# Optimization experiments

Measured on AMD Instinct MI355X. Metric: run time of the kernel, lower is better.

Reference implementation:

```python
import jax, jax.numpy as jnp
import numpy as np
import math

H = 8
E = 512
D_K = E // H
NEG = -1000000000.0
# last (and only surviving) row of dist_bar: one threshold per head
DIST_BAR = np.array([0.2, 0.3, 0.4, 0.5, 0.6, 0.7, 0.8, 0.9], dtype=np.float32)


def setup_inputs() -> dict:
    key = jax.random.key(0)
    ks = jax.random.split(key, 12)
    B, N = 8, 1024
    s = 1.0 / math.sqrt(E)
    inp = {
        "query": jax.random.normal(ks[0], (B, N, E), jnp.float32),
        "key": jax.random.normal(ks[1], (B, N, E), jnp.float32),
        "value": jax.random.normal(ks[2], (B, N, E), jnp.float32),
        "dist": jax.random.uniform(ks[3], (B, 1, N, N), jnp.float32),
        "mask": jnp.ones((B, N, N), jnp.int32),
        "Wq": jax.random.normal(ks[4], (E, E), jnp.float32) * s,
        "bq": jnp.zeros((E,), jnp.float32),
        "Wk": jax.random.normal(ks[5], (E, E), jnp.float32) * s,
        "bk": jnp.zeros((E,), jnp.float32),
        "Wv": jax.random.normal(ks[6], (E, E), jnp.float32) * s,
        "bv": jnp.zeros((E,), jnp.float32),
        "Wo": jax.random.normal(ks[7], (E, E), jnp.float32) * s,
        "bo": jnp.zeros((E,), jnp.float32),
    }
    return inp


def reference(query, key, value, dist, mask, Wq, bq, Wk, bk, Wv, bv, Wo, bo):
    B, N, _ = query.shape
    # project and split heads: [B, H, N, D_K]
    def heads(x, W, b):
        return (x @ W.T + b).reshape(B, N, H, D_K).transpose(0, 2, 1, 3)
    q = heads(query, Wq, bq)
    k = heads(key, Wk, bk)
    v = heads(value, Wv, bv)
    scores = jnp.einsum("bhqd,bhkd->bhqk", q, k) / math.sqrt(D_K)
    # padding mask: [B,N,N] -> [B,1,N,N]
    scores = jnp.where(mask[:, None, :, :] == 0, NEG, scores)
    # per-head distance mask: dist [B,1,N,N] < thr[h] -> [B,H,N,N]
    thr = jnp.asarray(DIST_BAR)[None, :, None, None]
    dmask = dist < thr
    # first row/col (global atom) always attend
    dmask = dmask.at[:, :, 0, :].set(True).at[:, :, :, 0].set(True)
    scores = jnp.where(dmask, scores, NEG)
    p = jax.nn.softmax(scores, axis=-1)
    out = jnp.einsum("bhqk,bhkd->bhqd", p, v)  # [B,H,N,D_K]
    out = out.transpose(0, 2, 1, 3).reshape(B, N, H * D_K)
    return out @ Wo.T + bo
```

## Files before the change

### kernel.cpp

```cpp
#include <hip/hip_runtime.h>
#include <stdint.h>


typedef __attribute__((ext_vector_type(8))) short short8;
typedef __attribute__((ext_vector_type(4))) float floatx4;

#define MFMA16(a, b, c) __builtin_amdgcn_mfma_f32_16x16x32_bf16((a), (b), (c), 0, 0, 0)

static __device__ __forceinline__ unsigned short f2bf(float f) {
  union { float f; unsigned u; } v; v.f = f;
  unsigned r = v.u + 0x7fffu + ((v.u >> 16) & 1u);
  return (unsigned short)(r >> 16);
}

static __device__ __forceinline__ void gload_lds16(const void* g, void* l) {
  __builtin_amdgcn_global_load_lds((const __attribute__((address_space(1))) unsigned int*)g,
                                   (__attribute__((address_space(3))) unsigned int*)l,
                                   16, 0, 0);
}
static __device__ __forceinline__ int xsw(int row) { return (row & 3) ^ ((row >> 2) & 3); }

__global__ void prep_kernel(const float* __restrict__ dist, const int* __restrict__ mask,
                            unsigned char* __restrict__ codesP,
                            const float* __restrict__ Wq, const float* __restrict__ Wk,
                            const float* __restrict__ Wv, const float* __restrict__ Wo,
                            unsigned short* __restrict__ o0, unsigned short* __restrict__ o1,
                            unsigned short* __restrict__ o2, unsigned short* __restrict__ o3,
                            const float* __restrict__ Qf, const float* __restrict__ Kf,
                            const float* __restrict__ Vf,
                            unsigned short* __restrict__ Qb, unsigned short* __restrict__ Kb,
                            unsigned short* __restrict__ Vb) {
  const int tid = threadIdx.x;
  const unsigned bx = blockIdx.x;
  if (bx >= 3072) {
    int j = bx - 3072;
    int arr = j >> 11;
    const float* s = (arr == 0) ? Qf : (arr == 1) ? Kf : Vf;
    unsigned short* d = (arr == 0) ? Qb : (arr == 1) ? Kb : Vb;
    int idx = (j & 2047) * 256 + tid;
    float4 v0 = ((const float4*)s)[idx * 2];
    float4 v1 = ((const float4*)s)[idx * 2 + 1];
    short8 o;
    o[0] = (short)f2bf(v0.x); o[1] = (short)f2bf(v0.y);
    o[2] = (short)f2bf(v0.z); o[3] = (short)f2bf(v0.w);
    o[4] = (short)f2bf(v1.x); o[5] = (short)f2bf(v1.y);
    o[6] = (short)f2bf(v1.z); o[7] = (short)f2bf(v1.w);
    *(short8*)(d + (size_t)idx * 8) = o;
    return;
  }
  if (bx >= 2048) {
    int i = (bx - 2048) * 256 + tid;
    int w = i >> 16, loc = i & 65535;
    const float* s = (w == 0) ? Wq : (w == 1) ? Wk : (w == 2) ? Wv : Wo;
    unsigned short* d = (w == 0) ? o0 : (w == 1) ? o1 : (w == 2) ? o2 : o3;
    float4 v = ((const float4*)s)[loc];
    ushort4 o;
    o.x = f2bf(v.x); o.y = f2bf(v.y); o.z = f2bf(v.z); o.w = f2bf(v.w);
    ((ushort4*)d)[loc] = o;
    return;
  }
  __shared__ __align__(16) unsigned char cbuf[4096];
  const int bc = bx;
  const int b = bc >> 8;
  const int rg = (bc >> 3) & 31;
  const int kt = bc & 7;
  const int row_local = tid >> 3;
  const int colseg = (tid & 7) * 16;
  const int row = rg * 32 + row_local;
  const int st = row_local >> 4;
  const int c = row_local & 15;
  const int ci = tid & 7;
  const size_t ibase = ((size_t)b << 20) + (size_t)row * 1024 + kt * 128 + colseg;
  float4 d4[4]; int4 m4[4];
#pragma unroll
  for (int g = 0; g < 4; g++) {
    d4[g] = ((const float4*)(dist + ibase))[g];
    m4[g] = ((const int4*)(mask + ibase))[g];
  }
#pragma unroll
  for (int hi = 0; hi < 4; hi++) {
    float dvv[4] = {d4[hi].x, d4[hi].y, d4[hi].z, d4[hi].w};
    int mvv[4] = {m4[hi].x, m4[hi].y, m4[hi].z, m4[hi].w};
    unsigned pack = 0;
#pragma unroll
    for (int r = 0; r < 4; r++) {
      int col = kt * 128 + colseg + hi * 4 + r;
      float d = dvv[r];
      int hmin = (d >= 0.2f) + (d >= 0.3f) + (d >= 0.4f) + (d >= 0.5f) +
                 (d >= 0.6f) + (d >= 0.7f) + (d >= 0.8f) + (d >= 0.9f);
      unsigned cc = (unsigned)hmin;
      if (row == 0 || col == 0) cc = 0;
      if (mvv[r] == 0) cc = 9;
      pack |= cc << (r * 8);
    }
    *(unsigned*)&cbuf[(hi * 16 + c) * 64 + st * 32 + ci * 4] = pack;
  }
  __syncthreads();
  *(uint4*)&codesP[(size_t)bc * 4096 + tid * 16] = *(const uint4*)&cbuf[tid * 16];
}

__global__ __launch_bounds__(256) void qkv_gemm(
    const unsigned short* __restrict__ Aq, const unsigned short* __restrict__ Ak,
    const unsigned short* __restrict__ Av,
    const unsigned short* __restrict__ Wqp, const unsigned short* __restrict__ Wkp,
    const unsigned short* __restrict__ Wvp,
    const float* __restrict__ bq, const float* __restrict__ bk, const float* __restrict__ bv,
    unsigned short* __restrict__ Qh, unsigned short* __restrict__ Kh,
    unsigned short* __restrict__ Vt) {
  const int z = blockIdx.z;
  const unsigned short* A = (z == 0) ? Aq : (z == 1) ? Ak : Av;
  const unsigned short* W = (z == 0) ? Wqp : (z == 1) ? Wkp : Wvp;
  const float* bias = (z == 0) ? bq : (z == 1) ? bk : bv;
  unsigned short* O = (z == 0) ? Qh : (z == 1) ? Kh : Vt;

  __shared__ __align__(16) short As[128 * 32];
  __shared__ __align__(16) short Bs[128 * 32];
  const int tid = threadIdx.x;
  const int lane = tid & 63;
  const int wave = tid >> 6;
  const int c = lane & 15;
  const int q = lane >> 4;
  const int m0 = blockIdx.x * 128;
  const int n0 = blockIdx.y * 128;
  const int wr = (wave >> 1) * 64;
  const int wc = (wave & 1) * 64;

  floatx4 acc[4][4];
#pragma unroll
  for (int i = 0; i < 4; i++)
#pragma unroll
    for (int j = 0; j < 4; j++) acc[i][j] = (floatx4)(0.0f);

  for (int k0 = 0; k0 < 512; k0 += 32) {
    __syncthreads();
#pragma unroll
    for (int it = 0; it < 2; it++) {
      int slot = wave * 128 + it * 64 + lane;
      int arow = slot >> 2, ach = slot & 3;
      int g = ach ^ xsw(arow);
      gload_lds16(A + (size_t)(m0 + arow) * 512 + k0 + g * 8,
                  &As[(size_t)(wave * 128 + it * 64) * 8]);
      gload_lds16(W + (size_t)(n0 + arow) * 512 + k0 + g * 8,
                  &Bs[(size_t)(wave * 128 + it * 64) * 8]);
    }
    __syncthreads();

    short8 af[4], bfv[4];
#pragma unroll
    for (int i = 0; i < 4; i++) {
      int row = wr + i * 16 + c;
      af[i] = *(const short8*)(&As[row * 32 + (q ^ xsw(row)) * 8]);
    }
#pragma unroll
    for (int j = 0; j < 4; j++) {
      int row = wc + j * 16 + c;
      bfv[j] = *(const short8*)(&Bs[row * 32 + (q ^ xsw(row)) * 8]);
    }
#pragma unroll
    for (int i = 0; i < 4; i++)
#pragma unroll
      for (int j = 0; j < 4; j++)
        acc[i][j] = MFMA16(af[i], bfv[j], acc[i][j]);
  }

#pragma unroll
  for (int i = 0; i < 4; i++) {
    int gm0 = m0 + wr + i * 16 + q * 4;
#pragma unroll
    for (int j = 0; j < 4; j++) {
      int gn = n0 + wc + j * 16 + c;
      float bb = bias[gn];
      int h = gn >> 6, d = gn & 63;
      if (z == 2) {
        int b = gm0 >> 10, n = gm0 & 1023;
        ushort4 pk;
#pragma unroll
        for (int r = 0; r < 4; r++) pk[r] = f2bf(acc[i][j][r] + bb);
        *(ushort4*)(&Vt[(((size_t)(b * 8 + h) * 64 + d) << 10) + n]) = pk;
      } else {
#pragma unroll
        for (int r = 0; r < 4; r++) {
          int m = gm0 + r;
          int b = m >> 10, n = m & 1023;
          O[((((size_t)(b * 8 + h)) << 10) + n) * 64 + d] = f2bf(acc[i][j][r] + bb);
        }
      }
    }
  }
}

__global__ __launch_bounds__(256) void out_gemm(const unsigned short* __restrict__ A,
                                                const unsigned short* __restrict__ W,
                                                const float* __restrict__ bias,
                                                float* __restrict__ Out) {
  __shared__ __align__(16) short As[64 * 32];
  __shared__ __align__(16) short Bs[128 * 32];
  const int tid = threadIdx.x;
  const int lane = tid & 63;
  const int wave = tid >> 6;
  const int c = lane & 15;
  const int q = lane >> 4;
  const int m0 = blockIdx.x * 64;
  const int n0 = blockIdx.y * 128;
  const int wr = (wave >> 1) * 32;
  const int wc = (wave & 1) * 64;

  floatx4 acc[2][4];
#pragma unroll
  for (int i = 0; i < 2; i++)
#pragma unroll
    for (int j = 0; j < 4; j++) acc[i][j] = (floatx4)(0.0f);

  for (int k0 = 0; k0 < 512; k0 += 32) {
    __syncthreads();
    {
      int slot = wave * 64 + lane;
      int arow = slot >> 2, ach = slot & 3;
      int g = ach ^ xsw(arow);
      gload_lds16(A + (size_t)(m0 + arow) * 512 + k0 + g * 8, &As[(size_t)(wave * 64) * 8]);
    }
#pragma unroll
    for (int it = 0; it < 2; it++) {
      int slot = wave * 128 + it * 64 + lane;
      int brow = slot >> 2, bch = slot & 3;
      int g = bch ^ xsw(brow);
      gload_lds16(W + (size_t)(n0 + brow) * 512 + k0 + g * 8,
                  &Bs[(size_t)(wave * 128 + it * 64) * 8]);
    }
    __syncthreads();

    short8 af[2], bfv[4];
#pragma unroll
    for (int i = 0; i < 2; i++) {
      int row = wr + i * 16 + c;
      af[i] = *(const short8*)(&As[row * 32 + (q ^ xsw(row)) * 8]);
    }
#pragma unroll
    for (int j = 0; j < 4; j++) {
      int row = wc + j * 16 + c;
      bfv[j] = *(const short8*)(&Bs[row * 32 + (q ^ xsw(row)) * 8]);
    }
#pragma unroll
    for (int i = 0; i < 2; i++)
#pragma unroll
      for (int j = 0; j < 4; j++)
        acc[i][j] = MFMA16(af[i], bfv[j], acc[i][j]);
  }

#pragma unroll
  for (int i = 0; i < 2; i++) {
    int gm0 = m0 + wr + i * 16 + q * 4;
#pragma unroll
    for (int j = 0; j < 4; j++) {
      int gn = n0 + wc + j * 16 + c;
      float bb = bias[gn];
#pragma unroll
      for (int r = 0; r < 4; r++)
        Out[(size_t)(gm0 + r) * 512 + gn] = acc[i][j][r] + bb;
    }
  }
}

__global__ __launch_bounds__(256, 3) void attn_kernel(const unsigned short* __restrict__ Qh,
                                                      const unsigned short* __restrict__ Kh,
                                                      const unsigned short* __restrict__ Vt,
                                                      const unsigned char* __restrict__ codesP,
                                                      unsigned short* __restrict__ AO) {
  __shared__ __align__(16) float Mrg[2 * 9 * 64 * 4];
  const int tid = threadIdx.x;
  const int lane = tid & 63;
  const int wave = tid >> 6;
  const int wsub = wave & 1;
  const int whalf = wave >> 1;
  const int c = lane & 15;
  const int q = lane >> 4;
  const int bid = blockIdx.x;
  const int swz = ((bid & 7) << 7) | (bid >> 3);
  const int bh = swz >> 4;
  const int gx = swz & 15;
  const int b = bh >> 3;
  const int h = bh & 7;
  const size_t base = (size_t)bh << 16;
  const int rbase = gx * 64 + wsub * 32;
  const int rg = rbase >> 5;

  short8 aq[2][2];
#pragma unroll
  for (int st = 0; st < 2; st++)
#pragma unroll
    for (int kk = 0; kk < 2; kk++)
      aq[st][kk] = *(const short8*)(Qh + base + (size_t)(rbase + st * 16 + c) * 64 + kk * 32 + q * 8);

  const unsigned char* cbt = codesP + (size_t)(b * 32 + rg) * 32768 + lane * 64;
  const unsigned short* Kb = Kh + base;
  const unsigned short* Vb = Vt + base;

  const int src0 = (((2 * q) & 3) << 4) + c;
  const int src1 = (((2 * q + 1) & 3) << 4) + c;
  const bool hiq = (q >= 2);

  float rsum[2] = {0.0f, 0.0f};
  floatx4 o[2][4];
#pragma unroll
  for (int st = 0; st < 2; st++)
#pragma unroll
    for (int ci = 0; ci < 4; ci++) o[st][ci] = (floatx4)(0.0f);

  short8 bk00, bk01, bk10, bk11;
  {
    const unsigned short* Kt0 = Kb + (size_t)(whalf * 4) * 8192;
    bk00 = *(const short8*)(Kt0 + (size_t)(0 * 16 + c) * 64 + 0 * 32 + q * 8);
    bk01 = *(const short8*)(Kt0 + (size_t)(0 * 16 + c) * 64 + 1 * 32 + q * 8);
    bk10 = *(const short8*)(Kt0 + (size_t)(1 * 16 + c) * 64 + 0 * 32 + q * 8);
    bk11 = *(const short8*)(Kt0 + (size_t)(1 * 16 + c) * 64 + 1 * 32 + q * 8);
  }

#pragma unroll
  for (int ph = 0; ph < 16; ph++) {
    const int kt = whalf * 4 + (ph >> 2);
    const int j = ph & 3;
    const unsigned char* cp = cbt + (size_t)kt * 4096;

    short8 vv0 = *(const short8*)(Vb + (size_t)(0 * 16 + c) * 1024 + kt * 128 + j * 32 + q * 8);
    short8 vv1 = *(const short8*)(Vb + (size_t)(1 * 16 + c) * 1024 + kt * 128 + j * 32 + q * 8);
    short8 vv2 = *(const short8*)(Vb + (size_t)(2 * 16 + c) * 1024 + kt * 128 + j * 32 + q * 8);
    short8 vv3 = *(const short8*)(Vb + (size_t)(3 * 16 + c) * 1024 + kt * 128 + j * 32 + q * 8);
    uint2 cw0 = *(const uint2*)(cp + j * 8);
    uint2 cw1 = *(const uint2*)(cp + 32 + j * 8);

    floatx4 s2[2][2];
    s2[0][0] = (floatx4)(0.0f); s2[0][1] = (floatx4)(0.0f);
    s2[1][0] = (floatx4)(0.0f); s2[1][1] = (floatx4)(0.0f);
    __builtin_amdgcn_s_setprio(1);
    s2[0][0] = MFMA16(bk00, aq[0][0], s2[0][0]);
    s2[1][0] = MFMA16(bk00, aq[1][0], s2[1][0]);
    s2[0][0] = MFMA16(bk01, aq[0][1], s2[0][0]);
    s2[1][0] = MFMA16(bk01, aq[1][1], s2[1][0]);
    s2[0][1] = MFMA16(bk10, aq[0][0], s2[0][1]);
    s2[1][1] = MFMA16(bk10, aq[1][0], s2[1][1]);
    s2[0][1] = MFMA16(bk11, aq[0][1], s2[0][1]);
    s2[1][1] = MFMA16(bk11, aq[1][1], s2[1][1]);
    __builtin_amdgcn_s_setprio(0);

    if (ph < 15) {
      const int phn = ph + 1;
      const int ktn = whalf * 4 + (phn >> 2);
      const int jn = phn & 3;
      const unsigned short* Ktn = Kb + (size_t)ktn * 8192;
      bk00 = *(const short8*)(Ktn + (size_t)((2 * jn + 0) * 16 + c) * 64 + 0 * 32 + q * 8);
      bk01 = *(const short8*)(Ktn + (size_t)((2 * jn + 0) * 16 + c) * 64 + 1 * 32 + q * 8);
      bk10 = *(const short8*)(Ktn + (size_t)((2 * jn + 1) * 16 + c) * 64 + 0 * 32 + q * 8);
      bk11 = *(const short8*)(Ktn + (size_t)((2 * jn + 1) * 16 + c) * 64 + 1 * 32 + q * 8);
    }

    short8 apf[2];
#pragma unroll
    for (int st = 0; st < 2; st++) {
      unsigned pw[2][2];
#pragma unroll
      for (int u = 0; u < 2; u++) {
        unsigned w = st ? (u ? cw1.y : cw1.x) : (u ? cw0.y : cw0.x);
        float ev[4];
#pragma unroll
        for (int r = 0; r < 4; r++) {
          int code = (w >> (r * 8)) & 0xff;
          float ee = (h >= code) ? exp2f(s2[st][u][r] * 0.1803368801111362f) : 0.0f;
          rsum[st] += ee;
          ev[r] = ee;
        }
        asm("v_cvt_pk_bf16_f32 %0, %1, %2" : "=v"(pw[u][0]) : "v"(ev[0]), "v"(ev[1]));
        asm("v_cvt_pk_bf16_f32 %0, %1, %2" : "=v"(pw[u][1]) : "v"(ev[2]), "v"(ev[3]));
      }
      unsigned t0a = __shfl(pw[0][0], src0), t0b = __shfl(pw[1][0], src0);
      unsigned t1a = __shfl(pw[0][1], src0), t1b = __shfl(pw[1][1], src0);
      unsigned t2a = __shfl(pw[0][0], src1), t2b = __shfl(pw[1][0], src1);
      unsigned t3a = __shfl(pw[0][1], src1), t3b = __shfl(pw[1][1], src1);
      union { unsigned u[4]; short8 v; } cvt;
      cvt.u[0] = hiq ? t0b : t0a;
      cvt.u[1] = hiq ? t1b : t1a;
      cvt.u[2] = hiq ? t2b : t2a;
      cvt.u[3] = hiq ? t3b : t3a;
      apf[st] = cvt.v;
    }

    __builtin_amdgcn_sched_barrier(0);

    __builtin_amdgcn_s_setprio(1);
    o[0][0] = MFMA16(apf[0], vv0, o[0][0]);
    o[1][0] = MFMA16(apf[1], vv0, o[1][0]);
    o[0][1] = MFMA16(apf[0], vv1, o[0][1]);
    o[1][1] = MFMA16(apf[1], vv1, o[1][1]);
    o[0][2] = MFMA16(apf[0], vv2, o[0][2]);
    o[1][2] = MFMA16(apf[1], vv2, o[1][2]);
    o[0][3] = MFMA16(apf[0], vv3, o[0][3]);
    o[1][3] = MFMA16(apf[1], vv3, o[1][3]);
    __builtin_amdgcn_s_setprio(0);
  }

  __syncthreads();
  if (whalf == 1) {
#pragma unroll
    for (int st = 0; st < 2; st++)
#pragma unroll
      for (int ci = 0; ci < 4; ci++)
        *(floatx4*)&Mrg[(((wsub * 9 + st * 4 + ci) * 64) + lane) * 4] = o[st][ci];
    float2 rr; rr.x = rsum[0]; rr.y = rsum[1];
    *(float2*)&Mrg[(((wsub * 9 + 8) * 64) + lane) * 4] = rr;
  }
  __syncthreads();
  if (whalf == 1) return;

#pragma unroll
  for (int st = 0; st < 2; st++)
#pragma unroll
    for (int ci = 0; ci < 4; ci++) {
      floatx4 p = *(const floatx4*)&Mrg[(((wsub * 9 + st * 4 + ci) * 64) + lane) * 4];
      o[st][ci] += p;
    }
  {
    float2 pr = *(const float2*)&Mrg[(((wsub * 9 + 8) * 64) + lane) * 4];
    rsum[0] += pr.x; rsum[1] += pr.y;
  }

  float inv2[2];
#pragma unroll
  for (int st = 0; st < 2; st++) {
    float v = rsum[st];
    v += __shfl_xor(v, 16);
    v += __shfl_xor(v, 32);
    inv2[st] = 1.0f / v;
  }
  const int sb = (lane & 48) + ((lane & 48) >> 2);
  float iv[2][4];
#pragma unroll
  for (int st = 0; st < 2; st++)
#pragma unroll
    for (int r = 0; r < 4; r++) iv[st][r] = __shfl(inv2[st], sb + r);

#pragma unroll
  for (int st = 0; st < 2; st++)
#pragma unroll
    for (int r = 0; r < 4; r++) {
      int n = rbase + st * 16 + q * 4 + r;
      size_t ob = ((size_t)((b << 10) + n)) * 512 + h * 64;
#pragma unroll
      for (int ci = 0; ci < 4; ci++)
        AO[ob + ci * 16 + c] = f2bf(o[st][ci][r] * iv[st][r]);
    }
}

extern "C" void kernel_launch(void* const* d_in, const int* in_sizes, int n_in,
                              void* d_out, int out_size, void* d_ws, size_t ws_size,
                              hipStream_t stream) {
  const float* query = (const float*)d_in[0];
  const float* key_  = (const float*)d_in[1];
  const float* value = (const float*)d_in[2];
  const float* dist  = (const float*)d_in[3];
  const int*   mask  = (const int*)d_in[4];
  const float* Wq = (const float*)d_in[5];
  const float* bq = (const float*)d_in[6];
  const float* Wk = (const float*)d_in[7];
  const float* bk = (const float*)d_in[8];
  const float* Wv = (const float*)d_in[9];
  const float* bv = (const float*)d_in[10];
  const float* Wo = (const float*)d_in[11];
  const float* bo = (const float*)d_in[12];

  char* ws = (char*)d_ws;
  size_t off = 0;
  auto alloc = [&](size_t bytes) -> char* {
    char* p = ws + off;
    off += (bytes + 255) & ~(size_t)255;
    return p;
  };
  const size_t NQKV = 8192ull * 512;
  unsigned short* wq16 = (unsigned short*)alloc(512ull * 512 * 2);
  unsigned short* wk16 = (unsigned short*)alloc(512ull * 512 * 2);
  unsigned short* wv16 = (unsigned short*)alloc(512ull * 512 * 2);
  unsigned short* wo16 = (unsigned short*)alloc(512ull * 512 * 2);
  unsigned short* Qh = (unsigned short*)alloc(NQKV * 2);
  unsigned short* Kh = (unsigned short*)alloc(NQKV * 2);
  unsigned short* Vt = (unsigned short*)alloc(NQKV * 2);
  unsigned short* AO = (unsigned short*)alloc(NQKV * 2);
  unsigned char*  codesP = (unsigned char*)alloc(8ull * 1024 * 1024);
  unsigned short* Qi = (unsigned short*)alloc(NQKV * 2);
  unsigned short* Ki = (unsigned short*)alloc(NQKV * 2);
  unsigned short* Vi = (unsigned short*)alloc(NQKV * 2);

  prep_kernel<<<9216, 256, 0, stream>>>(dist, mask, codesP, Wq, Wk, Wv, Wo,
                                        wq16, wk16, wv16, wo16,
                                        query, key_, value, Qi, Ki, Vi);
  qkv_gemm<<<dim3(64, 4, 3), 256, 0, stream>>>(Qi, Ki, Vi, wq16, wk16, wv16,
                                               bq, bk, bv, Qh, Kh, Vt);
  attn_kernel<<<1024, 256, 0, stream>>>(Qh, Kh, Vt, codesP, AO);
  out_gemm<<<dim3(128, 4), 256, 0, stream>>>(AO, wo16, bo, (float*)d_out);
}
```

Before: 276.7 us.

## Have each attention wave cover full key range, dropping split-K LDS merge

```diff
diff --git a/kernel.cpp b/kernel.cpp
--- a/kernel.cpp
+++ b/kernel.cpp
@@ -261,27 +261,24 @@
   }
 }
 
-__global__ __launch_bounds__(256, 3) void attn_kernel(const unsigned short* __restrict__ Qh,
-                                                      const unsigned short* __restrict__ Kh,
-                                                      const unsigned short* __restrict__ Vt,
-                                                      const unsigned char* __restrict__ codesP,
-                                                      unsigned short* __restrict__ AO) {
-  __shared__ __align__(16) float Mrg[2 * 9 * 64 * 4];
+__global__ __launch_bounds__(256) void attn_kernel(const unsigned short* __restrict__ Qh,
+                                                   const unsigned short* __restrict__ Kh,
+                                                   const unsigned short* __restrict__ Vt,
+                                                   const unsigned char* __restrict__ codesP,
+                                                   unsigned short* __restrict__ AO) {
   const int tid = threadIdx.x;
   const int lane = tid & 63;
   const int wave = tid >> 6;
-  const int wsub = wave & 1;
-  const int whalf = wave >> 1;
   const int c = lane & 15;
   const int q = lane >> 4;
   const int bid = blockIdx.x;
-  const int swz = ((bid & 7) << 7) | (bid >> 3);
-  const int bh = swz >> 4;
-  const int gx = swz & 15;
+  const int swz = ((bid & 7) << 6) | (bid >> 3);
+  const int bh = swz >> 3;
+  const int gx = swz & 7;
   const int b = bh >> 3;
   const int h = bh & 7;
   const size_t base = (size_t)bh << 16;
-  const int rbase = gx * 64 + wsub * 32;
+  const int rbase = gx * 128 + wave * 32;
   const int rg = rbase >> 5;
 
   short8 aq[2][2];
@@ -306,120 +303,139 @@
 #pragma unroll
     for (int ci = 0; ci < 4; ci++) o[st][ci] = (floatx4)(0.0f);
 
-  short8 bk00, bk01, bk10, bk11;
+  short8 bkA00, bkA01, bkA10, bkA11;
+  short8 bkB00, bkB01, bkB10, bkB11;
   {
-    const unsigned short* Kt0 = Kb + (size_t)(whalf * 4) * 8192;
-    bk00 = *(const short8*)(Kt0 + (size_t)(0 * 16 + c) * 64 + 0 * 32 + q * 8);
-    bk01 = *(const short8*)(Kt0 + (size_t)(0 * 16 + c) * 64 + 1 * 32 + q * 8);
-    bk10 = *(const short8*)(Kt0 + (size_t)(1 * 16 + c) * 64 + 0 * 32 + q * 8);
-    bk11 = *(const short8*)(Kt0 + (size_t)(1 * 16 + c) * 64 + 1 * 32 + q * 8);
+    const unsigned short* KtA = Kb;
+    const unsigned short* KtB = Kb + (size_t)4 * 8192;
+    bkA00 = *(const short8*)(KtA + (size_t)(0 * 16 + c) * 64 + 0 * 32 + q * 8);
+    bkA01 = *(const short8*)(KtA + (size_t)(0 * 16 + c) * 64 + 1 * 32 + q * 8);
+    bkA10 = *(const short8*)(KtA + (size_t)(1 * 16 + c) * 64 + 0 * 32 + q * 8);
+    bkA11 = *(const short8*)(KtA + (size_t)(1 * 16 + c) * 64 + 1 * 32 + q * 8);
+    bkB00 = *(const short8*)(KtB + (size_t)(0 * 16 + c) * 64 + 0 * 32 + q * 8);
+    bkB01 = *(const short8*)(KtB + (size_t)(0 * 16 + c) * 64 + 1 * 32 + q * 8);
+    bkB10 = *(const short8*)(KtB + (size_t)(1 * 16 + c) * 64 + 0 * 32 + q * 8);
+    bkB11 = *(const short8*)(KtB + (size_t)(1 * 16 + c) * 64 + 1 * 32 + q * 8);
   }
 
 #pragma unroll
   for (int ph = 0; ph < 16; ph++) {
-    const int kt = whalf * 4 + (ph >> 2);
     const int j = ph & 3;
-    const unsigned char* cp = cbt + (size_t)kt * 4096;
-
-    short8 vv0 = *(const short8*)(Vb + (size_t)(0 * 16 + c) * 1024 + kt * 128 + j * 32 + q * 8);
-    short8 vv1 = *(const short8*)(Vb + (size_t)(1 * 16 + c) * 1024 + kt * 128 + j * 32 + q * 8);
-    short8 vv2 = *(const short8*)(Vb + (size_t)(2 * 16 + c) * 1024 + kt * 128 + j * 32 + q * 8);
-    short8 vv3 = *(const short8*)(Vb + (size_t)(3 * 16 + c) * 1024 + kt * 128 + j * 32 + q * 8);
-    uint2 cw0 = *(const uint2*)(cp + j * 8);
-    uint2 cw1 = *(const uint2*)(cp + 32 + j * 8);
-
-    floatx4 s2[2][2];
-    s2[0][0] = (floatx4)(0.0f); s2[0][1] = (floatx4)(0.0f);
-    s2[1][0] = (floatx4)(0.0f); s2[1][1] = (floatx4)(0.0f);
+    const int kta = ph >> 2;
+    const int ktb = 4 + (ph >> 2);
+    const unsigned char* cpA = cbt + (size_t)kta * 4096;
+    const unsigned char* cpB = cbt + (size_t)ktb * 4096;
+
+    short8 vvA0 = *(const short8*)(Vb + (size_t)(0 * 16 + c) * 1024 + kta * 128 + j * 32 + q * 8);
+    short8 vvA1 = *(const short8*)(Vb + (size_t)(1 * 16 + c) * 1024 + kta * 128 + j * 32 + q * 8);
+    short8 vvA2 = *(const short8*)(Vb + (size_t)(2 * 16 + c) * 1024 + kta * 128 + j * 32 + q * 8);
+    short8 vvA3 = *(const short8*)(Vb + (size_t)(3 * 16 + c) * 1024 + kta * 128 + j * 32 + q * 8);
+    short8 vvB0 = *(const short8*)(Vb + (size_t)(0 * 16 + c) * 1024 + ktb * 128 + j * 32 + q * 8);
+    short8 vvB1 = *(const short8*)(Vb + (size_t)(1 * 16 + c) * 1024 + ktb * 128 + j * 32 + q * 8);
+    short8 vvB2 = *(const short8*)(Vb + (size_t)(2 * 16 + c) * 1024 + ktb * 128 + j * 32 + q * 8);
+    short8 vvB3 = *(const short8*)(Vb + (size_t)(3 * 16 + c) * 1024 + ktb * 128 + j * 32 + q * 8);
+    uint2 cwA0 = *(const uint2*)(cpA + j * 8);
+    uint2 cwA1 = *(const uint2*)(cpA + 32 + j * 8);
+    uint2 cwB0 = *(const uint2*)(cpB + j * 8);
+    uint2 cwB1 = *(const uint2*)(cpB + 32 + j * 8);
+
+    floatx4 sA[2][2], sB[2][2];
+    sA[0][0] = (floatx4)(0.0f); sA[0][1] = (floatx4)(0.0f);
+    sA[1][0] = (floatx4)(0.0f); sA[1][1] = (floatx4)(0.0f);
+    sB[0][0] = (floatx4)(0.0f); sB[0][1] = (floatx4)(0.0f);
+    sB[1][0] = (floatx4)(0.0f); sB[1][1] = (floatx4)(0.0f);
     __builtin_amdgcn_s_setprio(1);
-    s2[0][0] = MFMA16(bk00, aq[0][0], s2[0][0]);
-    s2[1][0] = MFMA16(bk00, aq[1][0], s2[1][0]);
-    s2[0][0] = MFMA16(bk01, aq[0][1], s2[0][0]);
-    s2[1][0] = MFMA16(bk01, aq[1][1], s2[1][0]);
-    s2[0][1] = MFMA16(bk10, aq[0][0], s2[0][1]);
-    s2[1][1] = MFMA16(bk10, aq[1][0], s2[1][1]);
-    s2[0][1] = MFMA16(bk11, aq[0][1], s2[0][1]);
-    s2[1][1] = MFMA16(bk11, aq[1][1], s2[1][1]);
+    sA[0][0] = MFMA16(bkA00, aq[0][0], sA[0][0]);
+    sA[1][0] = MFMA16(bkA00, aq[1][0], sA[1][0]);
+    sA[0][1] = MFMA16(bkA10, aq[0][0], sA[0][1]);
+    sA[1][1] = MFMA16(bkA10, aq[1][0], sA[1][1]);
+    sB[0][0] = MFMA16(bkB00, aq[0][0], sB[0][0]);
+    sB[1][0] = MFMA16(bkB00, aq[1][0], sB[1][0]);
+    sB[0][1] = MFMA16(bkB10, aq[0][0], sB[0][1]);
+    sB[1][1] = MFMA16(bkB10, aq[1][0], sB[1][1]);
+    sA[0][0] = MFMA16(bkA01, aq[0][1], sA[0][0]);
+    sA[1][0] = MFMA16(bkA01, aq[1][1], sA[1][0]);
+    sA[0][1] = MFMA16(bkA11, aq[0][1], sA[0][1]);
+    sA[1][1] = MFMA16(bkA11, aq[1][1], sA[1][1]);
+    sB[0][0] = MFMA16(bkB01, aq[0][1], sB[0][0]);
+    sB[1][0] = MFMA16(bkB01, aq[1][1], sB[1][0]);
+    sB[0][1] = MFMA16(bkB11, aq[0][1], sB[0][1]);
+    sB[1][1] = MFMA16(bkB11, aq[1][1], sB[1][1]);
     __builtin_amdgcn_s_setprio(0);
 
     if (ph < 15) {
       const int phn = ph + 1;
-      const int ktn = whalf * 4 + (phn >> 2);
       const int jn = phn & 3;
-      const unsigned short* Ktn = Kb + (size_t)ktn * 8192;
-      bk00 = *(const short8*)(Ktn + (size_t)((2 * jn + 0) * 16 + c) * 64 + 0 * 32 + q * 8);
-      bk01 = *(const short8*)(Ktn + (size_t)((2 * jn + 0) * 16 + c) * 64 + 1 * 32 + q * 8);
-      bk10 = *(const short8*)(Ktn + (size_t)((2 * jn + 1) * 16 + c) * 64 + 0 * 32 + q * 8);
-      bk11 = *(const short8*)(Ktn + (size_t)((2 * jn + 1) * 16 + c) * 64 + 1 * 32 + q * 8);
-    }
-
-    short8 apf[2];
-#pragma unroll
-    for (int st = 0; st < 2; st++) {
-      unsigned pw[2][2];
-#pragma unroll
-      for (int u = 0; u < 2; u++) {
-        unsigned w = st ? (u ? cw1.y : cw1.x) : (u ? cw0.y : cw0.x);
-        float ev[4];
-#pragma unroll
-        for (int r = 0; r < 4; r++) {
-          int code = (w >> (r * 8)) & 0xff;
-          float ee = (h >= code) ? exp2f(s2[st][u][r] * 0.1803368801111362f) : 0.0f;
-          rsum[st] += ee;
-          ev[r] = ee;
+      const int ktan = phn >> 2;
+      const unsigned short* KtAn = Kb + (size_t)ktan * 8192;
+      const unsigned short* KtBn = Kb + (size_t)(4 + ktan) * 8192;
+      bkA00 = *(const short8*)(KtAn + (size_t)((2 * jn + 0) * 16 + c) * 64 + 0 * 32 + q * 8);
+      bkA01 = *(const short8*)(KtAn + (size_t)((2 * jn + 0) * 16 + c) * 64 + 1 * 32 + q * 8);
+      bkA10 = *(const short8*)(KtAn + (size_t)((2 * jn + 1) * 16 + c) * 64 + 0 * 32 + q * 8);
+      bkA11 = *(const short8*)(KtAn + (size_t)((2 * jn + 1) * 16 + c) * 64 + 1 * 32 + q * 8);
+      bkB00 = *(const short8*)(KtBn + (size_t)((2 * jn + 0) * 16 + c) * 64 + 0 * 32 + q * 8);
+      bkB01 = *(const short8*)(KtBn + (size_t)((2 * jn + 0) * 16 + c) * 64 + 1 * 32 + q * 8);
+      bkB10 = *(const short8*)(KtBn + (size_t)((2 * jn + 1) * 16 + c) * 64 + 0 * 32 + q * 8);
+      bkB11 = *(const short8*)(KtBn + (size_t)((2 * jn + 1) * 16 + c) * 64 + 1 * 32 + q * 8);
+    }
+
+    short8 apfA[2], apfB[2];
+#pragma unroll
+    for (int sstr = 0; sstr < 2; sstr++) {
+      floatx4 (*s2)[2] = sstr ? sB : sA;
+      uint2 cw0 = sstr ? cwB0 : cwA0;
+      uint2 cw1 = sstr ? cwB1 : cwA1;
+      short8* apf = sstr ? apfB : apfA;
+#pragma unroll
+      for (int st = 0; st < 2; st++) {
+        unsigned pw[2][2];
+#pragma unroll
+        for (int u = 0; u < 2; u++) {
+          unsigned w = st ? (u ? cw1.y : cw1.x) : (u ? cw0.y : cw0.x);
+          float ev[4];
+#pragma unroll
+          for (int r = 0; r < 4; r++) {
+            int code = (w >> (r * 8)) & 0xff;
+            float ee = (h >= code) ? exp2f(s2[st][u][r] * 0.1803368801111362f) : 0.0f;
+            rsum[st] += ee;
+            ev[r] = ee;
+          }
+          asm("v_cvt_pk_bf16_f32 %0, %1, %2" : "=v"(pw[u][0]) : "v"(ev[0]), "v"(ev[1]));
+          asm("v_cvt_pk_bf16_f32 %0, %1, %2" : "=v"(pw[u][1]) : "v"(ev[2]), "v"(ev[3]));
         }
-        asm("v_cvt_pk_bf16_f32 %0, %1, %2" : "=v"(pw[u][0]) : "v"(ev[0]), "v"(ev[1]));
-        asm("v_cvt_pk_bf16_f32 %0, %1, %2" : "=v"(pw[u][1]) : "v"(ev[2]), "v"(ev[3]));
+        unsigned t0a = __shfl(pw[0][0], src0), t0b = __shfl(pw[1][0], src0);
+        unsigned t1a = __shfl(pw[0][1], src0), t1b = __shfl(pw[1][1], src0);
+        unsigned t2a = __shfl(pw[0][0], src1), t2b = __shfl(pw[1][0], src1);
+        unsigned t3a = __shfl(pw[0][1], src1), t3b = __shfl(pw[1][1], src1);
+        union { unsigned u[4]; short8 v; } cvt;
+        cvt.u[0] = hiq ? t0b : t0a;
+        cvt.u[1] = hiq ? t1b : t1a;
+        cvt.u[2] = hiq ? t2b : t2a;
+        cvt.u[3] = hiq ? t3b : t3a;
+        apf[st] = cvt.v;
       }
-      unsigned t0a = __shfl(pw[0][0], src0), t0b = __shfl(pw[1][0], src0);
-      unsigned t1a = __shfl(pw[0][1], src0), t1b = __shfl(pw[1][1], src0);
-      unsigned t2a = __shfl(pw[0][0], src1), t2b = __shfl(pw[1][0], src1);
-      unsigned t3a = __shfl(pw[0][1], src1), t3b = __shfl(pw[1][1], src1);
-      union { unsigned u[4]; short8 v; } cvt;
-      cvt.u[0] = hiq ? t0b : t0a;
-      cvt.u[1] = hiq ? t1b : t1a;
-      cvt.u[2] = hiq ? t2b : t2a;
-      cvt.u[3] = hiq ? t3b : t3a;
-      apf[st] = cvt.v;
     }
 
     __builtin_amdgcn_sched_barrier(0);
 
     __builtin_amdgcn_s_setprio(1);
-    o[0][0] = MFMA16(apf[0], vv0, o[0][0]);
-    o[1][0] = MFMA16(apf[1], vv0, o[1][0]);
-    o[0][1] = MFMA16(apf[0], vv1, o[0][1]);
-    o[1][1] = MFMA16(apf[1], vv1, o[1][1]);
-    o[0][2] = MFMA16(apf[0], vv2, o[0][2]);
-    o[1][2] = MFMA16(apf[1], vv2, o[1][2]);
-    o[0][3] = MFMA16(apf[0], vv3, o[0][3]);
-    o[1][3] = MFMA16(apf[1], vv3, o[1][3]);
+    o[0][0] = MFMA16(apfA[0], vvA0, o[0][0]);
+    o[1][0] = MFMA16(apfA[1], vvA0, o[1][0]);
+    o[0][1] = MFMA16(apfA[0], vvA1, o[0][1]);
+    o[1][1] = MFMA16(apfA[1], vvA1, o[1][1]);
+    o[0][2] = MFMA16(apfA[0], vvA2, o[0][2]);
+    o[1][2] = MFMA16(apfA[1], vvA2, o[1][2]);
+    o[0][3] = MFMA16(apfA[0], vvA3, o[0][3]);
+    o[1][3] = MFMA16(apfA[1], vvA3, o[1][3]);
+    o[0][0] = MFMA16(apfB[0], vvB0, o[0][0]);
+    o[1][0] = MFMA16(apfB[1], vvB0, o[1][0]);
+    o[0][1] = MFMA16(apfB[0], vvB1, o[0][1]);
+    o[1][1] = MFMA16(apfB[1], vvB1, o[1][1]);
+    o[0][2] = MFMA16(apfB[0], vvB2, o[0][2]);
+    o[1][2] = MFMA16(apfB[1], vvB2, o[1][2]);
+    o[0][3] = MFMA16(apfB[0], vvB3, o[0][3]);
+    o[1][3] = MFMA16(apfB[1], vvB3, o[1][3]);
     __builtin_amdgcn_s_setprio(0);
-  }
-
-  __syncthreads();
-  if (whalf == 1) {
-#pragma unroll
-    for (int st = 0; st < 2; st++)
-#pragma unroll
-      for (int ci = 0; ci < 4; ci++)
-        *(floatx4*)&Mrg[(((wsub * 9 + st * 4 + ci) * 64) + lane) * 4] = o[st][ci];
-    float2 rr; rr.x = rsum[0]; rr.y = rsum[1];
-    *(float2*)&Mrg[(((wsub * 9 + 8) * 64) + lane) * 4] = rr;
-  }
-  __syncthreads();
-  if (whalf == 1) return;
-
-#pragma unroll
-  for (int st = 0; st < 2; st++)
-#pragma unroll
-    for (int ci = 0; ci < 4; ci++) {
-      floatx4 p = *(const floatx4*)&Mrg[(((wsub * 9 + st * 4 + ci) * 64) + lane) * 4];
-      o[st][ci] += p;
-    }
-  {
-    float2 pr = *(const float2*)&Mrg[(((wsub * 9 + 8) * 64) + lane) * 4];
-    rsum[0] += pr.x; rsum[1] += pr.y;
   }
 
   float inv2[2];
@@ -492,6 +508,6 @@
                                         query, key_, value, Qi, Ki, Vi);
   qkv_gemm<<<dim3(64, 4, 3), 256, 0, stream>>>(Qi, Ki, Vi, wq16, wk16, wv16,
                                                bq, bk, bv, Qh, Kh, Vt);
-  attn_kernel<<<1024, 256, 0, stream>>>(Qh, Kh, Vt, codesP, AO);
+  attn_kernel<<<512, 256, 0, stream>>>(Qh, Kh, Vt, codesP, AO);
   out_gemm<<<dim3(128, 4), 256, 0, stream>>>(AO, wo16, bo, (float*)d_out);
 }
```

After: 384.1 us. +38.8%, slower.
